# Kernel optimization log

Measured on AMD Instinct MI355X. Metric: run time of the kernel, lower is better.

## Reference

```python
import jax, jax.numpy as jnp
import numpy as np

MAX_STEP = 4
G_HID = 16      # hidden_graph_num
S_HID = 10      # hidden_graph_size
D = 128         # embed_dim / hidden_dim
N = 100000      # total nodes across batch of session graphs
E = 640000      # total edges
B = 2048        # number of graphs (fixed num_segments)
VOCAB = 100000  # POI vocabulary
NEG_SLOPE = 0.01  # LeakyReLU default


def leaky(x):
    return jnp.where(x >= 0, x, NEG_SLOPE * x)


def setup_inputs() -> dict:
    key = jax.random.key(0)
    ks = jax.random.split(key, 10)
    x_idx = jax.random.randint(ks[0], (N,), 0, VOCAB)
    edge_index = jax.random.randint(ks[1], (2, E), 0, N)
    batch = jnp.sort(jax.random.randint(ks[2], (N,), 0, B))
    poi_emb = jax.random.normal(ks[3], (VOCAB, D), jnp.float32) * 0.02
    fc_w = jax.random.normal(ks[4], (D, D), jnp.float32) / np.sqrt(D)
    fc_b = jnp.zeros((D,), jnp.float32)
    hidden_adj = jax.random.normal(ks[5], (G_HID, S_HID * (S_HID - 1) // 2), jnp.float32)
    hidden_feat = jax.random.normal(ks[6], (G_HID, S_HID, D), jnp.float32)
    mlp_w = jax.random.normal(ks[7], (G_HID * MAX_STEP, D), jnp.float32) / np.sqrt(G_HID * MAX_STEP)
    mlp_b = jnp.zeros((D,), jnp.float32)
    return dict(x_idx=x_idx, edge_index=edge_index, batch=batch,
                poi_emb=poi_emb, fc_w=fc_w, fc_b=fc_b,
                hidden_adj=hidden_adj, hidden_feat=hidden_feat,
                mlp_w=mlp_w, mlp_b=mlp_b)


def reference(x_idx, edge_index, batch, poi_emb, fc_w, fc_b,
              hidden_adj, hidden_feat, mlp_w, mlp_b):
    # Symmetric hidden-graph adjacency from upper-triangular params
    iu, ju = np.triu_indices(S_HID, 1)
    A = jnp.zeros((G_HID, S_HID, S_HID), hidden_adj.dtype).at[:, iu, ju].set(leaky(hidden_adj))
    A = A + jnp.swapaxes(A, 1, 2)

    # Node features: embedding lookup -> Linear -> sigmoid  [N, D]
    x = jax.nn.sigmoid(poi_emb[x_idx] @ fc_w + fc_b)
    z = hidden_feat                                   # [G, S, D]
    zx = jnp.einsum('gsd,nd->gsn', z, x)              # [G, S, N]

    src, dst = edge_index[0], edge_index[1]
    outs = []
    for i in range(MAX_STEP):
        if i == 0:
            # eye @ z == z, so t == zx (faithful to the torch einsum chain)
            t = zx
        else:
            # MessagePassing.propagate with default add aggregation:
            # x_new[v] = sum_{(u->v) in E} x[u]
            x = jax.ops.segment_sum(x[src], dst, num_segments=N)
            z = jnp.einsum('gst,gtd->gsd', A, z)
            t = jnp.einsum('gsd,nd->gsn', z, x)
        t = zx * t                                    # dropout = identity (eval)
        # graph-wise scatter pooling: index_add over node axis -> [B, G, S]
        pooled = jax.ops.segment_sum(jnp.moveaxis(t, 2, 0), batch, num_segments=B)
        outs.append(pooled.sum(axis=2))               # [B, G]

    out = jnp.concatenate(outs, axis=1)               # [B, G*MAX_STEP]
    return leaky(out @ mlp_w + mlp_b)                 # [B, D]
```

## Files before the change

### kernel.cpp

```cpp
#include <hip/hip_runtime.h>
#include <hip/hip_bf16.h>
#include <math.h>

#define G_HID 16
#define S_HID 10
#define D 128
#define MAX_STEP 4
#define NEG 0.01f
#define SCAN_TILE 1024
#define YT_PITCH 168

typedef __attribute__((ext_vector_type(8))) short short8;
typedef __attribute__((ext_vector_type(4))) float f32x4;

__device__ __forceinline__ float leaky_f(float v){ return v >= 0.f ? v : NEG*v; }
__device__ __forceinline__ unsigned short f2bf(float f){
    unsigned int u = __float_as_uint(f);
    u = (u + 0x7FFFu + ((u>>16)&1u)) >> 16;
    return (unsigned short)u;
}
__device__ __forceinline__ float bf_lo(unsigned int v){ return __uint_as_float(v << 16); }
__device__ __forceinline__ float bf_hi(unsigned int v){ return __uint_as_float(v & 0xFFFF0000u); }
__device__ __forceinline__ float bfu(unsigned short u){ return __uint_as_float(((unsigned int)u) << 16); }

__global__ void prep_kernel(const float* __restrict__ hidden_adj,
                            const float* __restrict__ hidden_feat,
                            short* __restrict__ zpack,
                            float* __restrict__ Ai)
{
    int g = blockIdx.x;
    __shared__ float Ag[S_HID][S_HID];
    __shared__ float A2[S_HID][S_HID];
    __shared__ float A3[S_HID][S_HID];
    int t = threadIdx.x;
    if (t < S_HID*S_HID) {
        int i = t / S_HID, j = t % S_HID;
        float v = 0.f;
        if (i < j) {
            int idx = 9*i - i*(i-1)/2 + (j - i - 1);
            v = leaky_f(hidden_adj[g*45 + idx]);
        } else if (i > j) {
            int idx = 9*j - j*(j-1)/2 + (i - j - 1);
            v = leaky_f(hidden_adj[g*45 + idx]);
        }
        Ag[i][j] = v;
    }
    __syncthreads();
    if (t < 100){
        int s = t/10, u = t%10;
        float c = 0.f;
        #pragma unroll
        for (int w = 0; w < 10; ++w) c += Ag[s][w]*Ag[w][u];
        A2[s][u] = c;
    }
    __syncthreads();
    if (t < 100){
        int s = t/10, u = t%10;
        float c = 0.f;
        #pragma unroll
        for (int w = 0; w < 10; ++w) c += A2[s][w]*Ag[w][u];
        A3[s][u] = c;
        Ai[0*1600 + g*100 + t] = Ag[s][u];
        Ai[1*1600 + g*100 + t] = A2[s][u];
        Ai[2*1600 + g*100 + t] = A3[s][u];
    }
    for (int idx = t; idx < S_HID*D; idx += 128) {
        int s = idx / D, k = idx % D;
        int row = g*S_HID + s;
        int tt = row >> 4, li = row & 15;
        int kt = k >> 5, q = (k >> 3) & 3, j = k & 7;
        zpack[((tt*4 + kt)*64 + q*16 + li)*8 + j] = (short)f2bf(hidden_feat[(g*S_HID + s)*D + k]);
    }
}

__global__ void wpack_kernel(const float* __restrict__ fc_w, short* __restrict__ wp){
    int idx = blockIdx.x*256 + threadIdx.x;
    if (idx >= 16384) return;
    int j = idx & 7, lane = (idx >> 3) & 63, ctkt = idx >> 9;
    int ct = ctkt & 7, kt = ctkt >> 3;
    int k   = kt*32 + (lane >> 4)*8 + j;
    int col = ct*16 + (lane & 15);
    wp[idx] = (short)f2bf(fc_w[k*D + col]);
}

__global__ void count_kernel(const int* __restrict__ dst, int* __restrict__ offsets,
                             int* __restrict__ rnk, int E){
    int e = blockIdx.x*blockDim.x + threadIdx.x;
    if (e < E) rnk[e] = atomicAdd(&offsets[dst[e]+1], 1);
}

__global__ void scan1_kernel(int* __restrict__ data, int* __restrict__ bsums, int n){
    __shared__ int wsum[4];
    int base = blockIdx.x * SCAN_TILE + threadIdx.x*4;
    int v[4];
    #pragma unroll
    for (int j=0;j<4;++j) v[j] = (base+j < n) ? data[base+j] : 0;
    v[1]+=v[0]; v[2]+=v[1]; v[3]+=v[2];
    int lane = threadIdx.x & 63;
    int w = threadIdx.x >> 6;
    int s = v[3];
    for (int d=1; d<64; d<<=1){
        int o = __shfl_up(s, d);
        if (lane >= d) s += o;
    }
    if (lane == 63) wsum[w] = s;
    int sexc = s - v[3];
    __syncthreads();
    int woff = 0;
    for (int ww=0; ww<w; ++ww) woff += wsum[ww];
    int off = woff + sexc;
    #pragma unroll
    for (int j=0;j<4;++j) { if (base+j < n) data[base+j] = v[j] + off; }
    if (threadIdx.x == 255) bsums[blockIdx.x] = off + v[3];
}

__global__ void scan2_kernel(int* __restrict__ bsums, int nb){
    __shared__ int ws[4];
    __shared__ int carry_s;
    if (threadIdx.x == 0) carry_s = 0;
    __syncthreads();
    for (int start = 0; start < nb; start += 256){
        int i = start + (int)threadIdx.x;
        int v = (i < nb) ? bsums[i] : 0;
        int lane = threadIdx.x & 63, w = threadIdx.x >> 6;
        int s = v;
        for (int d=1; d<64; d<<=1){ int o = __shfl_up(s, d); if (lane >= d) s += o; }
        if (lane == 63) ws[w] = s;
        __syncthreads();
        int woff = 0;
        for (int ww=0; ww<w; ++ww) woff += ws[ww];
        int inc = s + woff + carry_s;
        if (i < nb) bsums[i] = inc - v;
        __syncthreads();
        if (threadIdx.x == 255) carry_s = inc;
        __syncthreads();
    }
}

__global__ void scan3_kernel(int* __restrict__ data, const int* __restrict__ bsums, int n){
    int base = blockIdx.x * SCAN_TILE + threadIdx.x*4;
    int add = bsums[blockIdx.x];
    #pragma unroll
    for (int j=0;j<4;++j){ if (base+j < n) data[base+j] += add; }
}

__global__ void fill_kernel(const int* __restrict__ src, const int* __restrict__ dst,
                            const int* __restrict__ rnk, const int* __restrict__ offsets,
                            int* __restrict__ csr, int E){
    int e = blockIdx.x*blockDim.x + threadIdx.x;
    if (e < E) csr[offsets[dst[e]] + rnk[e]] = src[e];
}

__device__ __forceinline__ void compute_slots(const int* __restrict__ batch, int n0, int N,
                                              int* slots, int* slotb, int* nslots_s, int t){
    if (t < 64) {
        int gn = n0 + t;
        int b = (gn < N) ? batch[gn] : -1;
        int bprev = -1;
        if (t > 0) bprev = (gn-1 < N) ? batch[gn-1] : -1;
        int flag = (t == 0 || b != bprev) ? 1 : 0;
        int s = flag;
        for (int d=1; d<64; d<<=1){ int o = __shfl_up(s, d); if (t >= d) s += o; }
        int slot = s - 1;
        slots[t] = slot;
        if (flag) slotb[slot] = b;
        if (t == 63) *nslots_s = s;
    }
}

__global__ __launch_bounds__(256) void embed_step0_kernel(
        const int* __restrict__ x_idx, const float* __restrict__ poi_emb,
        const short* __restrict__ wp, const float* __restrict__ fc_b,
        const short* __restrict__ zpack, const int* __restrict__ batch,
        unsigned short* __restrict__ W0,
        float* __restrict__ pooled, int N)
{
    __shared__ __align__(16) char lbuf[64*YT_PITCH*2];
    __shared__ float accs[64][G_HID];
    __shared__ int slots[64];
    __shared__ int slotb[64];
    __shared__ int nslots_s;
    unsigned short* xs  = (unsigned short*)lbuf;
    unsigned short* ytr = (unsigned short*)lbuf;
    int n0 = blockIdx.x * 64;
    int t = threadIdx.x;

    #pragma unroll
    for (int i = 0; i < 8; ++i) {
        int idx = t + i*256;
        int row = idx >> 5, c4 = (idx & 31)*4;
        int gn = n0 + row;
        float4 v = make_float4(0.f,0.f,0.f,0.f);
        if (gn < N) v = *reinterpret_cast<const float4*>(&poi_emb[(size_t)x_idx[gn]*D + c4]);
        unsigned int p0 = (unsigned int)f2bf(v.x) | ((unsigned int)f2bf(v.y) << 16);
        unsigned int p1 = (unsigned int)f2bf(v.z) | ((unsigned int)f2bf(v.w) << 16);
        *reinterpret_cast<uint2*>(&xs[row*136 + c4]) = make_uint2(p0, p1);
    }
    for (int idx = t; idx < 64*G_HID; idx += 256) ((float*)accs)[idx] = 0.f;
    compute_slots(batch, n0, N, slots, slotb, &nslots_s, t);
    __syncthreads();

    int l = t & 63, w = t >> 6, li = l & 15, q = l >> 4;
    short8 a[4];
    #pragma unroll
    for (int kt = 0; kt < 4; ++kt)
        a[kt] = *reinterpret_cast<const short8*>(&xs[(w*16 + li)*136 + kt*32 + q*8]);
    f32x4 facc[8];
    #pragma unroll
    for (int ct = 0; ct < 8; ++ct) facc[ct] = (f32x4){0.f,0.f,0.f,0.f};
    #pragma unroll
    for (int kt = 0; kt < 4; ++kt){
        #pragma unroll
        for (int ct = 0; ct < 8; ++ct){
            short8 b = reinterpret_cast<const short8*>(wp)[(kt*8 + ct)*64 + l];
            facc[ct] = __builtin_amdgcn_mfma_f32_16x16x32_bf16(a[kt], b, facc[ct], 0, 0, 0);
        }
    }
    #pragma unroll
    for (int ct = 0; ct < 8; ++ct){
        float bias = fc_b[ct*16 + li];
        #pragma unroll
        for (int r = 0; r < 4; ++r){
            int row = w*16 + q*4 + r;
            float s = (n0 + row < N) ? 1.f/(1.f + __expf(-(facc[ct][r] + bias))) : 0.f;
            xs[row*136 + ct*16 + li] = f2bf(s);
        }
    }
    __syncthreads();
    short8 bw[4];
    #pragma unroll
    for (int kt = 0; kt < 4; ++kt)
        bw[kt] = *reinterpret_cast<const short8*>(&xs[(w*16 + li)*136 + kt*32 + q*8]);
    __syncthreads();

    #pragma unroll
    for (int t10 = 0; t10 < 10; ++t10){
        f32x4 acc = (f32x4){0.f,0.f,0.f,0.f};
        #pragma unroll
        for (int kt = 0; kt < 4; ++kt){
            short8 az = *reinterpret_cast<const short8*>(&zpack[((t10*4 + kt)*64 + l)*8]);
            acc = __builtin_amdgcn_mfma_f32_16x16x32_bf16(az, bw[kt], acc, 0, 0, 0);
        }
        uint2 pk;
        pk.x = (unsigned int)f2bf(acc[0]) | ((unsigned int)f2bf(acc[1]) << 16);
        pk.y = (unsigned int)f2bf(acc[2]) | ((unsigned int)f2bf(acc[3]) << 16);
        *reinterpret_cast<uint2*>(&ytr[(w*16 + li)*YT_PITCH + t10*16 + q*4]) = pk;
    }
    __syncthreads();

    {
        int nd = t >> 2, part = t & 3, gn = n0 + nd;
        if (gn < N){
            const uint2* srcl = reinterpret_cast<const uint2*>(&ytr[nd*YT_PITCH + part*40]);
            uint2* dstg = reinterpret_cast<uint2*>(&W0[(size_t)gn*160 + part*40]);
            #pragma unroll
            for (int k2 = 0; k2 < 10; ++k2) dstg[k2] = srcl[k2];
        }
    }
    #pragma unroll
    for (int i = 0; i < 4; ++i){
        int nd2 = t & 63;
        int g = (t >> 6) + i*4;
        if (n0 + nd2 < N){
            float c = 0.f;
            #pragma unroll
            for (int s = 0; s < S_HID; ++s){
                float y = bfu(ytr[nd2*YT_PITCH + g*10 + s]);
                c += y*y;
            }
            atomicAdd(&accs[slots[nd2]][g], c);
        }
    }
    __syncthreads();
    int ns = nslots_s;
    for (int idx = t; idx < ns*G_HID; idx += 256){
        int j = idx >> 4, g = idx & 15;
        int b = slotb[j];
        if (b >= 0) atomicAdd(&pooled[(size_t)b*64 + g], accs[j][g]);
    }
}

__global__ __launch_bounds__(256) void propw_kernel(
        const uint2* __restrict__ Win, uint2* __restrict__ Wout,
        const uint2* __restrict__ Y0,
        const int* __restrict__ offsets, const int* __restrict__ csr,
        const float* __restrict__ Ai_g,
        const int* __restrict__ batch, float* __restrict__ pooled,
        int N, int stepoff)
{
    __shared__ float Aw[1600];
    __shared__ float ylds[4][160];
    __shared__ float gacc[4][16];
    int t = threadIdx.x;
    for (int idx = t; idx < 1600; idx += 256) Aw[idx] = Ai_g[idx];
    __syncthreads();

    int wv = t >> 6, l = t & 63;
    int v = blockIdx.x*4 + wv;
    if (v >= N) return;

    int beg = offsets[v], end = offsets[v+1];
    float a0=0.f, a1=0.f, a2=0.f, a3=0.f;
    for (int base = beg; base < end; base += 64){
        int cnt = min(64, end - base);
        int myu = (base + l < end) ? csr[base + l] : 0;
        int ei = 0;
        for (; ei + 4 <= cnt; ei += 4){
            int u0 = __shfl(myu, ei), u1 = __shfl(myu, ei+1);
            int u2 = __shfl(myu, ei+2), u3 = __shfl(myu, ei+3);
            uint2 w0 = make_uint2(0,0), w1 = w0, w2 = w0, w3 = w0;
            if (l < 40){
                w0 = Win[(size_t)u0*40 + l];
                w1 = Win[(size_t)u1*40 + l];
                w2 = Win[(size_t)u2*40 + l];
                w3 = Win[(size_t)u3*40 + l];
            }
            a0 += bf_lo(w0.x) + bf_lo(w1.x) + bf_lo(w2.x) + bf_lo(w3.x);
            a1 += bf_hi(w0.x) + bf_hi(w1.x) + bf_hi(w2.x) + bf_hi(w3.x);
            a2 += bf_lo(w0.y) + bf_lo(w1.y) + bf_lo(w2.y) + bf_lo(w3.y);
            a3 += bf_hi(w0.y) + bf_hi(w1.y) + bf_hi(w2.y) + bf_hi(w3.y);
        }
        for (; ei < cnt; ++ei){
            int u = __shfl(myu, ei);
            uint2 wv2 = make_uint2(0,0);
            if (l < 40) wv2 = Win[(size_t)u*40 + l];
            a0 += bf_lo(wv2.x); a1 += bf_hi(wv2.x);
            a2 += bf_lo(wv2.y); a3 += bf_hi(wv2.y);
        }
    }
    if (l < 40){
        uint2 o;
        o.x = (unsigned int)f2bf(a0) | ((unsigned int)f2bf(a1) << 16);
        o.y = (unsigned int)f2bf(a2) | ((unsigned int)f2bf(a3) << 16);
        Wout[(size_t)v*40 + l] = o;
        uint2 y = Y0[(size_t)v*40 + l];
        float4 yf;
        yf.x = bf_lo(y.x); yf.y = bf_hi(y.x); yf.z = bf_lo(y.y); yf.w = bf_hi(y.y);
        *reinterpret_cast<float4*>(&ylds[wv][l*4]) = yf;
    }
    if (l < 16) gacc[wv][l] = 0.f;
    __threadfence_block();

    if (l < 40){
        float aj[4] = {a0, a1, a2, a3};
        int idx0 = 4*l;
        int ga = idx0/10, gb = (idx0+3)/10;
        float c0 = 0.f, c1 = 0.f;
        #pragma unroll
        for (int j = 0; j < 4; ++j){
            int idx = idx0 + j;
            int g = idx/10, s = idx - g*10;
            float u0v = 0.f;
            #pragma unroll
            for (int tt = 0; tt < 10; ++tt)
                u0v += Aw[g*100 + s*10 + tt] * ylds[wv][g*10 + tt];
            float p = u0v * aj[j];
            if (g == ga) c0 += p; else c1 += p;
        }
        atomicAdd(&gacc[wv][ga], c0);
        if (gb != ga) atomicAdd(&gacc[wv][gb], c1);
    }
    __threadfence_block();
    if (l < 16){
        int b = batch[v];
        atomicAdd(&pooled[(size_t)b*64 + stepoff + l], gacc[wv][l]);
    }
}

__global__ void out_kernel(const float* __restrict__ pooled, const float* __restrict__ mlp_w,
                           const float* __restrict__ mlp_b, float* __restrict__ out, int B){
    __shared__ float row[64];
    int b = blockIdx.x;
    int t = threadIdx.x;
    if (t < 64) row[t] = pooled[(size_t)b*64 + t];
    __syncthreads();
    float acc = mlp_b[t];
    for (int j=0;j<64;++j) acc += row[j]*mlp_w[j*D + t];
    out[(size_t)b*D + t] = leaky_f(acc);
}

extern "C" void kernel_launch(void* const* d_in, const int* in_sizes, int n_in,
                              void* d_out, int out_size, void* d_ws, size_t ws_size,
                              hipStream_t stream)
{
    const int*   x_idx = (const int*)d_in[0];
    const int*   edge  = (const int*)d_in[1];
    const int*   batch = (const int*)d_in[2];
    const float* poi   = (const float*)d_in[3];
    const float* fc_w  = (const float*)d_in[4];
    const float* fc_b  = (const float*)d_in[5];
    const float* adj   = (const float*)d_in[6];
    const float* feat  = (const float*)d_in[7];
    const float* mlp_w = (const float*)d_in[8];
    const float* mlp_b = (const float*)d_in[9];
    float* out = (float*)d_out;

    int N = in_sizes[0];
    int E = in_sizes[1] / 2;
    int B = out_size / D;
    int sblk = (N + 63) / 64;
    size_t NP = (size_t)sblk * 64;

    char* p = (char*)d_ws;
    auto alloc = [&](size_t bytes)->char* {
        char* r = p;
        p += (bytes + 255) & ~(size_t)255;
        return r;
    };
    unsigned short* Y0 = (unsigned short*)alloc(NP*160*2);
    unsigned short* Wa = (unsigned short*)alloc(NP*160*2);
    unsigned short* Wb = (unsigned short*)alloc(NP*160*2);
    float* pooled      = (float*)alloc((size_t)B*64*4);
    short* zpack       = (short*)alloc((size_t)20480*2);
    short* wp          = (short*)alloc((size_t)16384*2);
    float* Ai          = (float*)alloc((size_t)3*1600*4);
    int*   offsets     = (int*)alloc((size_t)(N+1)*4);
    int*   rnk         = (int*)alloc((size_t)E*4);
    int*   csr         = (int*)alloc((size_t)E*4);
    int*   bsums       = (int*)alloc(4096);

    const int* srcp = edge;
    const int* dstp = edge + E;

    hipMemsetAsync(offsets, 0, (size_t)(N+1)*4, stream);
    hipMemsetAsync(pooled, 0, (size_t)B*64*4, stream);

    prep_kernel<<<G_HID, 128, 0, stream>>>(adj, feat, zpack, Ai);
    wpack_kernel<<<64, 256, 0, stream>>>(fc_w, wp);

    count_kernel<<<(E+255)/256, 256, 0, stream>>>(dstp, offsets, rnk, E);
    int scan_n = N + 1;
    int nblk = (scan_n + SCAN_TILE - 1) / SCAN_TILE;
    scan1_kernel<<<nblk, 256, 0, stream>>>(offsets, bsums, scan_n);
    scan2_kernel<<<1, 256, 0, stream>>>(bsums, nblk);
    scan3_kernel<<<nblk, 256, 0, stream>>>(offsets, bsums, scan_n);
    fill_kernel<<<(E+255)/256, 256, 0, stream>>>(srcp, dstp, rnk, offsets, csr, E);

    embed_step0_kernel<<<sblk, 256, 0, stream>>>(x_idx, poi, wp, fc_b, zpack, batch,
                                                 Y0, pooled, N);

    const unsigned short* win = Y0;
    unsigned short* bufs[2] = {Wa, Wb};
    for (int i = 1; i < MAX_STEP; ++i){
        unsigned short* wout = bufs[(i-1) & 1];
        propw_kernel<<<(N+3)/4, 256, 0, stream>>>(
            (const uint2*)win, (uint2*)wout, (const uint2*)Y0,
            offsets, csr, Ai + (size_t)(i-1)*1600, batch, pooled, N, i*G_HID);
        win = wout;
    }
    out_kernel<<<B, D, 0, stream>>>(pooled, mlp_w, mlp_b, out, B);
}
```

Measured before the change: 399.0 us.

## Precompute per-step A^k-transformed Y0 in step0, simplify propagation reduction

The step-0 kernel now precomputes U_k = A^k·Y0 for all three later steps and writes them to new global buffers, with W0 stored in an s-major, g-interleaved layout. The propagation kernel then drops the per-node 10x10 matvec, its shared-memory staging and block-level atomics, and reduces with wavefront shuffles that produce four group sums per lane. Count and fill kernels process four edges per thread with vectorized loads. The trade is an extra 3×N×160 bf16 of writes and reads against removing repeated matrix work and LDS traffic in each propagation step.

```diff
diff --git a/kernel.cpp b/kernel.cpp
--- a/kernel.cpp
+++ b/kernel.cpp
@@ -8,7 +8,7 @@
 #define MAX_STEP 4
 #define NEG 0.01f
 #define SCAN_TILE 1024
-#define YT_PITCH 168
+#define YT_PITCH 170
 
 typedef __attribute__((ext_vector_type(8))) short short8;
 typedef __attribute__((ext_vector_type(4))) float f32x4;
@@ -21,7 +21,6 @@
 }
 __device__ __forceinline__ float bf_lo(unsigned int v){ return __uint_as_float(v << 16); }
 __device__ __forceinline__ float bf_hi(unsigned int v){ return __uint_as_float(v & 0xFFFF0000u); }
-__device__ __forceinline__ float bfu(unsigned short u){ return __uint_as_float(((unsigned int)u) << 16); }
 
 __global__ void prep_kernel(const float* __restrict__ hidden_adj,
                             const float* __restrict__ hidden_feat,
@@ -31,7 +30,6 @@
     int g = blockIdx.x;
     __shared__ float Ag[S_HID][S_HID];
     __shared__ float A2[S_HID][S_HID];
-    __shared__ float A3[S_HID][S_HID];
     int t = threadIdx.x;
     if (t < S_HID*S_HID) {
         int i = t / S_HID, j = t % S_HID;
@@ -52,6 +50,7 @@
         #pragma unroll
         for (int w = 0; w < 10; ++w) c += Ag[s][w]*Ag[w][u];
         A2[s][u] = c;
+        Ai[0*1600 + g*100 + t] = Ag[s][u];
     }
     __syncthreads();
     if (t < 100){
@@ -59,10 +58,8 @@
         float c = 0.f;
         #pragma unroll
         for (int w = 0; w < 10; ++w) c += A2[s][w]*Ag[w][u];
-        A3[s][u] = c;
-        Ai[0*1600 + g*100 + t] = Ag[s][u];
         Ai[1*1600 + g*100 + t] = A2[s][u];
-        Ai[2*1600 + g*100 + t] = A3[s][u];
+        Ai[2*1600 + g*100 + t] = c;
     }
     for (int idx = t; idx < S_HID*D; idx += 128) {
         int s = idx / D, k = idx % D;
@@ -85,8 +82,18 @@
 
 __global__ void count_kernel(const int* __restrict__ dst, int* __restrict__ offsets,
                              int* __restrict__ rnk, int E){
-    int e = blockIdx.x*blockDim.x + threadIdx.x;
-    if (e < E) rnk[e] = atomicAdd(&offsets[dst[e]+1], 1);
+    int e0 = (blockIdx.x*blockDim.x + threadIdx.x)*4;
+    if (e0 >= E) return;
+    if (e0 + 4 <= E){
+        int4 d = *reinterpret_cast<const int4*>(&dst[e0]);
+        int r0 = atomicAdd(&offsets[d.x+1], 1);
+        int r1 = atomicAdd(&offsets[d.y+1], 1);
+        int r2 = atomicAdd(&offsets[d.z+1], 1);
+        int r3 = atomicAdd(&offsets[d.w+1], 1);
+        *reinterpret_cast<int4*>(&rnk[e0]) = make_int4(r0,r1,r2,r3);
+    } else {
+        for (int e = e0; e < E; ++e) rnk[e] = atomicAdd(&offsets[dst[e]+1], 1);
+    }
 }
 
 __global__ void scan1_kernel(int* __restrict__ data, int* __restrict__ bsums, int n){
@@ -147,8 +154,20 @@
 __global__ void fill_kernel(const int* __restrict__ src, const int* __restrict__ dst,
                             const int* __restrict__ rnk, const int* __restrict__ offsets,
                             int* __restrict__ csr, int E){
-    int e = blockIdx.x*blockDim.x + threadIdx.x;
-    if (e < E) csr[offsets[dst[e]] + rnk[e]] = src[e];
+    int e0 = (blockIdx.x*blockDim.x + threadIdx.x)*4;
+    if (e0 >= E) return;
+    if (e0 + 4 <= E){
+        int4 d = *reinterpret_cast<const int4*>(&dst[e0]);
+        int4 r = *reinterpret_cast<const int4*>(&rnk[e0]);
+        int4 s = *reinterpret_cast<const int4*>(&src[e0]);
+        int o0 = offsets[d.x], o1 = offsets[d.y], o2 = offsets[d.z], o3 = offsets[d.w];
+        csr[o0 + r.x] = s.x;
+        csr[o1 + r.y] = s.y;
+        csr[o2 + r.z] = s.z;
+        csr[o3 + r.w] = s.w;
+    } else {
+        for (int e = e0; e < E; ++e) csr[offsets[dst[e]] + rnk[e]] = src[e];
+    }
 }
 
 __device__ __forceinline__ void compute_slots(const int* __restrict__ batch, int n0, int N,
@@ -172,7 +191,9 @@
         const int* __restrict__ x_idx, const float* __restrict__ poi_emb,
         const short* __restrict__ wp, const float* __restrict__ fc_b,
         const short* __restrict__ zpack, const int* __restrict__ batch,
-        unsigned short* __restrict__ W0,
+        const float* __restrict__ Ai,
+        unsigned short* __restrict__ W0, unsigned short* __restrict__ U,
+        unsigned long long uslice,
         float* __restrict__ pooled, int N)
 {
     __shared__ __align__(16) char lbuf[64*YT_PITCH*2];
@@ -241,20 +262,55 @@
             short8 az = *reinterpret_cast<const short8*>(&zpack[((t10*4 + kt)*64 + l)*8]);
             acc = __builtin_amdgcn_mfma_f32_16x16x32_bf16(az, bw[kt], acc, 0, 0, 0);
         }
-        uint2 pk;
-        pk.x = (unsigned int)f2bf(acc[0]) | ((unsigned int)f2bf(acc[1]) << 16);
-        pk.y = (unsigned int)f2bf(acc[2]) | ((unsigned int)f2bf(acc[3]) << 16);
-        *reinterpret_cast<uint2*>(&ytr[(w*16 + li)*YT_PITCH + t10*16 + q*4]) = pk;
+        int base = (w*16 + li)*YT_PITCH + t10*16 + q*4;
+        *reinterpret_cast<unsigned int*>(&ytr[base])   =
+            (unsigned int)f2bf(acc[0]) | ((unsigned int)f2bf(acc[1]) << 16);
+        *reinterpret_cast<unsigned int*>(&ytr[base+2]) =
+            (unsigned int)f2bf(acc[2]) | ((unsigned int)f2bf(acc[3]) << 16);
     }
     __syncthreads();
 
     {
-        int nd = t >> 2, part = t & 3, gn = n0 + nd;
-        if (gn < N){
-            const uint2* srcl = reinterpret_cast<const uint2*>(&ytr[nd*YT_PITCH + part*40]);
-            uint2* dstg = reinterpret_cast<uint2*>(&W0[(size_t)gn*160 + part*40]);
-            #pragma unroll
-            for (int k2 = 0; k2 < 10; ++k2) dstg[k2] = srcl[k2];
+        int nd = t & 63, rq = t >> 6, gn2 = n0 + nd;
+        if (gn2 < N){
+            if (rq == 0){
+                unsigned int* wrow = reinterpret_cast<unsigned int*>(W0 + (size_t)gn2*160);
+                #pragma unroll
+                for (int s = 0; s < 10; ++s){
+                    #pragma unroll
+                    for (int gp = 0; gp < 8; ++gp){
+                        unsigned int lo = ytr[nd*YT_PITCH + (2*gp)*10 + s];
+                        unsigned int hi = ytr[nd*YT_PITCH + (2*gp+1)*10 + s];
+                        wrow[s*8 + gp] = lo | (hi << 16);
+                    }
+                }
+            } else {
+                const float* Aw = Ai + (size_t)(rq-1)*1600;
+                unsigned int* urow = reinterpret_cast<unsigned int*>(
+                    U + (size_t)(rq-1)*uslice + (size_t)gn2*160);
+                for (int gp = 0; gp < 8; ++gp){
+                    float ya[10], yb[10];
+                    #pragma unroll
+                    for (int tt = 0; tt < 5; ++tt){
+                        unsigned int pa = *reinterpret_cast<const unsigned int*>(
+                            &ytr[nd*YT_PITCH + (2*gp)*10 + 2*tt]);
+                        unsigned int pb = *reinterpret_cast<const unsigned int*>(
+                            &ytr[nd*YT_PITCH + (2*gp+1)*10 + 2*tt]);
+                        ya[2*tt] = bf_lo(pa); ya[2*tt+1] = bf_hi(pa);
+                        yb[2*tt] = bf_lo(pb); yb[2*tt+1] = bf_hi(pb);
+                    }
+                    #pragma unroll
+                    for (int s = 0; s < 10; ++s){
+                        float ua = 0.f, ub = 0.f;
+                        #pragma unroll
+                        for (int tt = 0; tt < 10; ++tt){
+                            ua += Aw[(2*gp)*100   + s*10 + tt] * ya[tt];
+                            ub += Aw[(2*gp+1)*100 + s*10 + tt] * yb[tt];
+                        }
+                        urow[s*8 + gp] = (unsigned int)f2bf(ua) | ((unsigned int)f2bf(ub) << 16);
+                    }
+                }
+            }
         }
     }
     #pragma unroll
@@ -265,7 +321,7 @@
             float c = 0.f;
             #pragma unroll
             for (int s = 0; s < S_HID; ++s){
-                float y = bfu(ytr[nd2*YT_PITCH + g*10 + s]);
+                float y = bf_lo((unsigned int)ytr[nd2*YT_PITCH + g*10 + s]);
                 c += y*y;
             }
             atomicAdd(&accs[slots[nd2]][g], c);
@@ -282,88 +338,65 @@
 
 __global__ __launch_bounds__(256) void propw_kernel(
         const uint2* __restrict__ Win, uint2* __restrict__ Wout,
-        const uint2* __restrict__ Y0,
+        const uint2* __restrict__ Ui,
         const int* __restrict__ offsets, const int* __restrict__ csr,
-        const float* __restrict__ Ai_g,
         const int* __restrict__ batch, float* __restrict__ pooled,
         int N, int stepoff)
 {
-    __shared__ float Aw[1600];
-    __shared__ float ylds[4][160];
-    __shared__ float gacc[4][16];
     int t = threadIdx.x;
-    for (int idx = t; idx < 1600; idx += 256) Aw[idx] = Ai_g[idx];
-    __syncthreads();
-
     int wv = t >> 6, l = t & 63;
     int v = blockIdx.x*4 + wv;
     if (v >= N) return;
-
     int beg = offsets[v], end = offsets[v+1];
+    int lc = min(l, 39);
     float a0=0.f, a1=0.f, a2=0.f, a3=0.f;
     for (int base = beg; base < end; base += 64){
         int cnt = min(64, end - base);
         int myu = (base + l < end) ? csr[base + l] : 0;
-        int ei = 0;
-        for (; ei + 4 <= cnt; ei += 4){
-            int u0 = __shfl(myu, ei), u1 = __shfl(myu, ei+1);
-            int u2 = __shfl(myu, ei+2), u3 = __shfl(myu, ei+3);
-            uint2 w0 = make_uint2(0,0), w1 = w0, w2 = w0, w3 = w0;
-            if (l < 40){
-                w0 = Win[(size_t)u0*40 + l];
-                w1 = Win[(size_t)u1*40 + l];
-                w2 = Win[(size_t)u2*40 + l];
-                w3 = Win[(size_t)u3*40 + l];
-            }
+        for (int ei = 0; ei < cnt; ei += 4){
+            int u0 = __shfl(myu, ei);
+            int u1 = __shfl(myu, (ei+1)&63);
+            int u2 = __shfl(myu, (ei+2)&63);
+            int u3 = __shfl(myu, (ei+3)&63);
+            uint2 w0 = Win[(size_t)u0*40 + lc];
+            uint2 w1 = Win[(size_t)u1*40 + lc];
+            uint2 w2 = Win[(size_t)u2*40 + lc];
+            uint2 w3 = Win[(size_t)u3*40 + lc];
+            if (ei+1 >= cnt){ w1.x = 0u; w1.y = 0u; }
+            if (ei+2 >= cnt){ w2.x = 0u; w2.y = 0u; }
+            if (ei+3 >= cnt){ w3.x = 0u; w3.y = 0u; }
             a0 += bf_lo(w0.x) + bf_lo(w1.x) + bf_lo(w2.x) + bf_lo(w3.x);
             a1 += bf_hi(w0.x) + bf_hi(w1.x) + bf_hi(w2.x) + bf_hi(w3.x);
             a2 += bf_lo(w0.y) + bf_lo(w1.y) + bf_lo(w2.y) + bf_lo(w3.y);
             a3 += bf_hi(w0.y) + bf_hi(w1.y) + bf_hi(w2.y) + bf_hi(w3.y);
         }
-        for (; ei < cnt; ++ei){
-            int u = __shfl(myu, ei);
-            uint2 wv2 = make_uint2(0,0);
-            if (l < 40) wv2 = Win[(size_t)u*40 + l];
-            a0 += bf_lo(wv2.x); a1 += bf_hi(wv2.x);
-            a2 += bf_lo(wv2.y); a3 += bf_hi(wv2.y);
-        }
-    }
-    if (l < 40){
+    }
+    uint2 uv = Ui[(size_t)v*40 + lc];
+    bool act = (l < 40);
+    float c0 = act ? a0*bf_lo(uv.x) : 0.f;
+    float c1 = act ? a1*bf_hi(uv.x) : 0.f;
+    float c2 = act ? a2*bf_lo(uv.y) : 0.f;
+    float c3 = act ? a3*bf_hi(uv.y) : 0.f;
+    if (act){
         uint2 o;
         o.x = (unsigned int)f2bf(a0) | ((unsigned int)f2bf(a1) << 16);
         o.y = (unsigned int)f2bf(a2) | ((unsigned int)f2bf(a3) << 16);
         Wout[(size_t)v*40 + l] = o;
-        uint2 y = Y0[(size_t)v*40 + l];
-        float4 yf;
-        yf.x = bf_lo(y.x); yf.y = bf_hi(y.x); yf.z = bf_lo(y.y); yf.w = bf_hi(y.y);
-        *reinterpret_cast<float4*>(&ylds[wv][l*4]) = yf;
-    }
-    if (l < 16) gacc[wv][l] = 0.f;
-    __threadfence_block();
-
-    if (l < 40){
-        float aj[4] = {a0, a1, a2, a3};
-        int idx0 = 4*l;
-        int ga = idx0/10, gb = (idx0+3)/10;
-        float c0 = 0.f, c1 = 0.f;
-        #pragma unroll
-        for (int j = 0; j < 4; ++j){
-            int idx = idx0 + j;
-            int g = idx/10, s = idx - g*10;
-            float u0v = 0.f;
-            #pragma unroll
-            for (int tt = 0; tt < 10; ++tt)
-                u0v += Aw[g*100 + s*10 + tt] * ylds[wv][g*10 + tt];
-            float p = u0v * aj[j];
-            if (g == ga) c0 += p; else c1 += p;
-        }
-        atomicAdd(&gacc[wv][ga], c0);
-        if (gb != ga) atomicAdd(&gacc[wv][gb], c1);
-    }
-    __threadfence_block();
-    if (l < 16){
+    }
+    #pragma unroll
+    for (int m = 4; m <= 32; m <<= 1){
+        c0 += __shfl_xor(c0, m);
+        c1 += __shfl_xor(c1, m);
+        c2 += __shfl_xor(c2, m);
+        c3 += __shfl_xor(c3, m);
+    }
+    if (l < 4){
         int b = batch[v];
-        atomicAdd(&pooled[(size_t)b*64 + stepoff + l], gacc[wv][l]);
+        float* pb = &pooled[(size_t)b*64 + stepoff + 4*l];
+        atomicAdd(pb+0, c0);
+        atomicAdd(pb+1, c1);
+        atomicAdd(pb+2, c2);
+        atomicAdd(pb+3, c3);
     }
 }
 
@@ -407,9 +440,10 @@
         p += (bytes + 255) & ~(size_t)255;
         return r;
     };
-    unsigned short* Y0 = (unsigned short*)alloc(NP*160*2);
+    unsigned short* W0 = (unsigned short*)alloc(NP*160*2);
     unsigned short* Wa = (unsigned short*)alloc(NP*160*2);
     unsigned short* Wb = (unsigned short*)alloc(NP*160*2);
+    unsigned short* U  = (unsigned short*)alloc((size_t)3*NP*160*2);
     float* pooled      = (float*)alloc((size_t)B*64*4);
     short* zpack       = (short*)alloc((size_t)20480*2);
     short* wp          = (short*)alloc((size_t)16384*2);
@@ -428,24 +462,26 @@
     prep_kernel<<<G_HID, 128, 0, stream>>>(adj, feat, zpack, Ai);
     wpack_kernel<<<64, 256, 0, stream>>>(fc_w, wp);
 
-    count_kernel<<<(E+255)/256, 256, 0, stream>>>(dstp, offsets, rnk, E);
+    count_kernel<<<(E/4 + 255)/256, 256, 0, stream>>>(dstp, offsets, rnk, E);
     int scan_n = N + 1;
     int nblk = (scan_n + SCAN_TILE - 1) / SCAN_TILE;
     scan1_kernel<<<nblk, 256, 0, stream>>>(offsets, bsums, scan_n);
     scan2_kernel<<<1, 256, 0, stream>>>(bsums, nblk);
     scan3_kernel<<<nblk, 256, 0, stream>>>(offsets, bsums, scan_n);
-    fill_kernel<<<(E+255)/256, 256, 0, stream>>>(srcp, dstp, rnk, offsets, csr, E);
+    fill_kernel<<<(E/4 + 255)/256, 256, 0, stream>>>(srcp, dstp, rnk, offsets, csr, E);
 
     embed_step0_kernel<<<sblk, 256, 0, stream>>>(x_idx, poi, wp, fc_b, zpack, batch,
-                                                 Y0, pooled, N);
-
-    const unsigned short* win = Y0;
+                                                 Ai, W0, U, (unsigned long long)(NP*160),
+                                                 pooled, N);
+
+    const unsigned short* win = W0;
     unsigned short* bufs[2] = {Wa, Wb};
     for (int i = 1; i < MAX_STEP; ++i){
         unsigned short* wout = bufs[(i-1) & 1];
         propw_kernel<<<(N+3)/4, 256, 0, stream>>>(
-            (const uint2*)win, (uint2*)wout, (const uint2*)Y0,
-            offsets, csr, Ai + (size_t)(i-1)*1600, batch, pooled, N, i*G_HID);
+            (const uint2*)win, (uint2*)wout,
+            (const uint2*)(U + (size_t)(i-1)*NP*160),
+            offsets, csr, batch, pooled, N, i*G_HID);
         win = wout;
     }
     out_kernel<<<B, D, 0, stream>>>(pooled, mlp_w, mlp_b, out, B);
```

After: 444.8 us. 1.11x slower.
